# Kernel tuning notes

Measured on AMD Instinct MI355X. Metric: run time of the kernel, lower is better.

## Reference

```python
import jax, jax.numpy as jnp
import numpy as np

CAD = 5          # cubes_around_atoms_dim (default)
RES = 1.0        # resolution (default)
SIGMA = 0.93     # gaussian sigma from Li et al. 2014
LATO = 2 * CAD + 1


def _cube_offsets():
    # (LATO^3, 3) integer offsets of the neighborhood cube, as float32
    g = jnp.arange(-CAD, CAD + 1, dtype=jnp.float32)
    return jnp.stack(jnp.meshgrid(g, g, g, indexing='ij'), axis=-1).reshape(-1, 3)


def _compute_boxsize(coords):
    # Mirrors the torch code's data-dependent box sizing (concrete values).
    c = np.asarray(coords)
    minm = np.trunc(c.min(axis=1) / RES).min(axis=0)   # (3,)
    maxc = c.reshape(-1, 3).max(axis=0)                # (3,)
    return tuple(int(np.ceil(maxc[d] / RES) - minm[d] + (2 * CAD + 1)) for d in range(3))


def _forward(coords, radius, channels, numberchannels, boxsize):
    B, N, _ = coords.shape
    cube = _cube_offsets()                                   # (K,3), K = LATO^3
    mincoords = jnp.trunc(jnp.min(coords, axis=1) / RES)     # (B,3)
    translation = (mincoords - CAD)[:, None, :]              # (B,1,3)
    coords_s = coords * (1.0 / RES) - translation            # (B,N,3) scaled coords
    radius_s = radius * (1.0 / RES)                          # (B,N)
    # torch uses coords_scaled.data -> detached discrete coordinates
    disc = jnp.trunc(jax.lax.stop_gradient(coords_s))        # (B,N,3)
    # voxel centers: disc + cube + 1 + 0.5*resolution
    centers = disc[:, :, None, :] + cube[None, None] + (1.0 + 0.5 * RES)  # (B,N,K,3)
    dist = jnp.linalg.norm(coords_s[:, :, None, :] - centers, axis=-1)    # (B,N,K)
    expo = -(dist ** 2) / (SIGMA ** 2 * radius_s[:, :, None] ** 2)
    # torch clamps exponent at 10 via masked_fill (never hit: expo <= 0)
    occ = jnp.exp(jnp.minimum(expo, 10.0))                   # (B,N,K)
    idx = (disc[:, :, None, :] + cube[None, None] + 1.0).astype(jnp.int32)  # (B,N,K,3)
    b_idx = jnp.broadcast_to(jnp.arange(B, dtype=jnp.int32)[:, None, None], occ.shape)
    c_idx = jnp.broadcast_to(channels[:, :, None].astype(jnp.int32), occ.shape)
    vol = jnp.zeros((B, numberchannels) + boxsize, dtype=coords.dtype)
    vol = vol.at[b_idx.ravel(), c_idx.ravel(),
                 idx[..., 0].ravel(), idx[..., 1].ravel(), idx[..., 2].ravel()].add(occ.ravel())
    return vol


def setup_inputs() -> dict:
    key = jax.random.key(0)
    k1, k2, k3 = jax.random.split(key, 3)
    B, N, C = 4, 6000, 8
    coords = jax.random.uniform(k1, (B, N, 3), dtype=jnp.float32) * 60.0   # Angstrom box
    radius = 1.2 + 0.8 * jax.random.uniform(k2, (B, N), dtype=jnp.float32)  # vdW-like radii
    channels = jax.random.randint(k3, (B, N), 0, C)
    return {"coords": coords, "radius": radius, "channels": channels, "numberchannels": C}


def reference(coords, radius, channels, numberchannels):
    boxsize = _compute_boxsize(coords)
    return _forward(coords, radius, channels, numberchannels, boxsize)
```

## Files before the change

### kernel.cpp

```cpp
#include <hip/hip_runtime.h>


#define CAD 5
#define LATO 11
#define KOFF 1331
#define SIGMA 0.93f
#define BFIX 4
#define CFIX 8

#define RX 8
#define RY 8
#define RZ 8
#define XSTR 65
#define XCH_C (8 * XSTR)
#define SAMAX 512
#define NBB_CAP 6144

#define WS_MIN   0
#define WS_MAX   12
#define WS_CHT   24
#define WS_OFFS  64
#define WS_PACK  (WS_OFFS + BFIX * CFIX * NBB_CAP + 64)

struct Geo {
    int bx, by, bz, nbx, nby, nbz, nbb, nrx, nry, nrz;
    float tr[BFIX][3];
};

__device__ __forceinline__ void derive_geo(const float* __restrict__ ws, Geo& g) {
    float box[3];
#pragma unroll
    for (int d = 0; d < 3; ++d) {
        float lo = 1e30f, hi = -1e30f;
#pragma unroll
        for (int b = 0; b < BFIX; ++b) {
            float mnb = truncf(ws[WS_MIN + b * 3 + d]);
            lo = fminf(lo, mnb);
            hi = fmaxf(hi, ws[WS_MAX + b * 3 + d]);
            g.tr[b][d] = mnb - (float)CAD;
        }
        box[d] = ceilf(hi) - lo + (float)(2 * CAD + 1);
    }
    g.bx = (int)box[0]; g.by = (int)box[1]; g.bz = (int)box[2];
    g.nbx = (g.bx + 3) >> 2; g.nby = (g.by + 3) >> 2; g.nbz = (g.bz + 3) >> 2;
    g.nbb = g.nbx * g.nby * g.nbz;
    g.nrx = (g.bx + RX - 1) / RX;
    g.nry = (g.by + RY - 1) / RY;
    g.nrz = (g.bz + RZ - 1) / RZ;
}

__global__ __launch_bounds__(256) void vx_minmax(const float* __restrict__ coords,
                                                 const int* __restrict__ channels,
                                                 int N, float* __restrict__ ws) {
    int b = blockIdx.x;
    const float* c = coords + (size_t)b * N * 3;
    int* wsI = (int*)ws;

    __shared__ int chc[CFIX];
    if (threadIdx.x < CFIX) chc[threadIdx.x] = 0;
    __syncthreads();

    float mn[3] = {1e30f, 1e30f, 1e30f};
    float mx[3] = {-1e30f, -1e30f, -1e30f};
    for (int i = threadIdx.x; i < N; i += 256) {
#pragma unroll
        for (int d = 0; d < 3; ++d) {
            float v = c[i * 3 + d];
            mn[d] = fminf(mn[d], v);
            mx[d] = fmaxf(mx[d], v);
        }
        atomicAdd(&chc[channels[(size_t)b * N + i] & 7], 1);
    }
#pragma unroll
    for (int off = 32; off >= 1; off >>= 1) {
#pragma unroll
        for (int d = 0; d < 3; ++d) {
            mn[d] = fminf(mn[d], __shfl_down(mn[d], off, 64));
            mx[d] = fmaxf(mx[d], __shfl_down(mx[d], off, 64));
        }
    }
    __shared__ float smn[4][3], smx[4][3];
    int wave = threadIdx.x >> 6;
    if ((threadIdx.x & 63) == 0) {
#pragma unroll
        for (int d = 0; d < 3; ++d) { smn[wave][d] = mn[d]; smx[wave][d] = mx[d]; }
    }
    __syncthreads();
    if (threadIdx.x == 0) {
#pragma unroll
        for (int d = 0; d < 3; ++d) {
            for (int w = 1; w < 4; ++w) {
                mn[d] = fminf(mn[d], smn[w][d]);
                mx[d] = fmaxf(mx[d], smx[w][d]);
            }
            ws[WS_MIN + b * 3 + d] = mn[d];
            ws[WS_MAX + b * 3 + d] = mx[d];
        }
    }
    if (threadIdx.x < CFIX) wsI[WS_CHT + b * CFIX + threadIdx.x] = chc[threadIdx.x];
}

__global__ __launch_bounds__(1024) void vx_bin(const float* __restrict__ coords,
                                               const float* __restrict__ radius,
                                               const int* __restrict__ channels,
                                               float* __restrict__ ws, int N) {
    int c = blockIdx.x;
    int b = blockIdx.y;
    Geo g;
    derive_geo(ws, g);
    int* wsI = (int*)ws;
    int nbb = g.nbb;
    int t = threadIdx.x;

    __shared__ int cnt[NBB_CAP];
    __shared__ int ssum[1024];

    for (int i = t; i < nbb; i += 1024) cnt[i] = 0;
    __syncthreads();

    const float* cb = coords + (size_t)b * N * 3;
    float trx = g.tr[b][0], try_ = g.tr[b][1], trz = g.tr[b][2];

    for (int i = t; i < N; i += 1024) {
        if ((channels[(size_t)b * N + i] & 7) != c) continue;
        float sx = cb[i * 3 + 0] - trx;
        float sy = cb[i * 3 + 1] - try_;
        float sz = cb[i * 3 + 2] - trz;
        int bin = ((((int)sx) >> 2) * g.nby + (((int)sy) >> 2)) * g.nbz + (((int)sz) >> 2);
        atomicAdd(&cnt[bin], 1);
    }
    __syncthreads();

    int base = t * 6;
    int v[6];
    int sum = 0;
#pragma unroll
    for (int k = 0; k < 6; ++k) {
        v[k] = sum;
        int idx = base + k;
        sum += (idx < nbb) ? cnt[idx] : 0;
    }
    ssum[t] = sum;
    __syncthreads();
    for (int off = 1; off < 1024; off <<= 1) {
        int x = (t >= off) ? ssum[t - off] : 0;
        __syncthreads();
        ssum[t] += x;
        __syncthreads();
    }
    int excl = ssum[t] - sum;

    int gbase = b * N;
    for (int cc = 0; cc < 8; ++cc)
        if (cc < c) gbase += wsI[WS_CHT + b * CFIX + cc];

    int tab = (b * CFIX + c) * nbb;
#pragma unroll
    for (int k = 0; k < 6; ++k) {
        int idx = base + k;
        if (idx < nbb) wsI[WS_OFFS + tab + idx] = gbase + excl + v[k];
    }
    __syncthreads();
#pragma unroll
    for (int k = 0; k < 6; ++k) {
        int idx = base + k;
        if (idx < nbb) cnt[idx] = gbase + excl + v[k];
    }
    if (b == BFIX - 1 && c == CFIX - 1 && t == 0)
        wsI[WS_OFFS + BFIX * CFIX * nbb] = BFIX * N;
    __syncthreads();

    float4* p4 = (float4*)(ws + WS_PACK);
    for (int i = t; i < N; i += 1024) {
        if ((channels[(size_t)b * N + i] & 7) != c) continue;
        float sx = cb[i * 3 + 0] - trx;
        float sy = cb[i * 3 + 1] - try_;
        float sz = cb[i * 3 + 2] - trz;
        int bin = ((((int)sx) >> 2) * g.nby + (((int)sy) >> 2)) * g.nbz + (((int)sz) >> 2);
        int pos = atomicAdd(&cnt[bin], 1);
        float r_ = radius[(size_t)b * N + i];
        float inv = -1.4426950408889634f / (SIGMA * SIGMA * r_ * r_);
        p4[pos] = make_float4(sx - 0.5f, sy - 0.5f, sz - 0.5f, inv);
    }
}

#define DECL2(c) float a##c##_0 = 0.f, a##c##_1 = 0.f;
#define ACC2(c) { a##c##_0 += e0; a##c##_1 += e1; }

#define BODYF(A, c)                                                           \
    {                                                                         \
        float ddz = A.z - fzs;                                                \
        if (fabsf(ddz + 0.5f) <= 6.5f) {                                      \
            float ddx = A.x - fvx;                                            \
            float ddy = A.y - fvy;                                            \
            float s2 = __builtin_fmaf(ddx, ddx, ddy * ddy);                   \
            float e0 =                                                        \
                __builtin_amdgcn_exp2f(__builtin_fmaf(ddz, ddz, s2) * A.w);   \
            ddz -= 1.f;                                                       \
            float e1 =                                                        \
                __builtin_amdgcn_exp2f(__builtin_fmaf(ddz, ddz, s2) * A.w);   \
            ACC2(c)                                                           \
        }                                                                     \
    }

#define SWEEP_CH(c)                                                           \
    {                                                                         \
        int jb = s_roff[(c) * ncolxy], je = s_roff[((c) + 1) * ncolxy];       \
        int j = jb;                                                           \
        for (; j + 3 < je; j += 4) {                                          \
            float4 A0 = sA[j], A1 = sA[j + 1], A2 = sA[j + 2], A3 = sA[j + 3];\
            BODYF(A0, c) BODYF(A1, c) BODYF(A2, c) BODYF(A3, c)               \
        }                                                                     \
        for (; j < je; ++j) { float4 A = sA[j]; BODYF(A, c) }                 \
    }

#define XW(c, s)                                                              \
    xch[(s) * XCH_C + (2 * wave + 0) * XSTR + lyx] = a##c##_0;                \
    xch[(s) * XCH_C + (2 * wave + 1) * XSTR + lyx] = a##c##_1;

__global__ __launch_bounds__(256) void vx_gather(
    const float* __restrict__ ws, float* __restrict__ out) {
    Geo g;
    derive_geo(ws, g);
    const int* wsI = (const int*)ws;
    const float4* __restrict__ pk4 = (const float4*)(ws + WS_PACK);
    int nbb = g.nbb;
    int nbb8 = nbb * CFIX;
    int nreg = g.nrx * g.nry * g.nrz;
    int b = blockIdx.y;
    int t = threadIdx.x;
    int wave = t >> 6, lane = t & 63;
    int lx = lane >> 3, ly = lane & 7;
    int lyx = ly * 8 + lx;

    __shared__ float4 sA[SAMAX];
    __shared__ float xch[4 * XCH_C];
    __shared__ int s_beg[208], s_roff[208];
    __shared__ int wtot[4];

    for (int reg = blockIdx.x; reg < nreg; reg += gridDim.x) {
        int rz = reg % g.nrz;
        int tmp = reg / g.nrz;
        int ry = tmp % g.nry;
        int rx = tmp / g.nry;
        int X0 = rx * RX, Y0 = ry * RY, Z0 = rz * RZ;
        int zs = Z0 + 2 * wave;

        float fvx = (float)(X0 + lx);
        float fvy = (float)(Y0 + ly);
        float fzs = (float)zs;

        DECL2(0) DECL2(1) DECL2(2) DECL2(3)
        DECL2(4) DECL2(5) DECL2(6) DECL2(7)

        int xb0 = max((X0 - 6) >> 2, 0), xb1 = min((X0 + 11) >> 2, g.nbx - 1);
        int yb0 = max((Y0 - 6) >> 2, 0), yb1 = min((Y0 + 11) >> 2, g.nby - 1);
        int zb0 = max((Z0 - 6) >> 2, 0), zb1 = min((Z0 + 11) >> 2, g.nbz - 1);
        int nyr = yb1 - yb0 + 1;
        int ncolxy = (xb1 - xb0 + 1) * nyr;
        int NR = ncolxy * CFIX;

        int len = 0, beg = 0;
        if (t < NR) {
            int ch = t / ncolxy;
            int col = t - ch * ncolxy;
            int xb = xb0 + col / nyr, yb = yb0 + col % nyr;
            int keyb = ch * nbb + (xb * g.nby + yb) * g.nbz;
            beg = wsI[WS_OFFS + b * nbb8 + keyb + zb0];
            len = wsI[WS_OFFS + b * nbb8 + keyb + zb1 + 1] - beg;
        }
        int incl = len;
#pragma unroll
        for (int off = 1; off < 64; off <<= 1) {
            int v = __shfl_up(incl, off, 64);
            if (lane >= off) incl += v;
        }
        if (lane == 63) wtot[wave] = incl;
        __syncthreads();
        int addb = 0;
        for (int w = 0; w < 4; ++w)
            if (w < wave) addb += wtot[w];
        incl += addb;
        int excl = incl - len;
        if (t < NR) {
            s_beg[t] = beg;
            s_roff[t + 1] = incl;
        }
        if (t == 0) s_roff[0] = 0;
        __syncthreads();
        int S = s_roff[NR];

        if (S <= SAMAX) {
            if (t < NR) {
                for (int e = 0; e < len; ++e)
                    sA[excl + e] = pk4[beg + e];
            }
            __syncthreads();
            SWEEP_CH(0) SWEEP_CH(1) SWEEP_CH(2) SWEEP_CH(3)
            SWEEP_CH(4) SWEEP_CH(5) SWEEP_CH(6) SWEEP_CH(7)
        } else {
            __syncthreads();
            for (int r2 = 0; r2 < NR; ++r2) {
                int bg = s_beg[r2];
                int ln = s_roff[r2 + 1] - s_roff[r2];
                int c = r2 / ncolxy;
                for (int e = 0; e < ln; ++e) {
                    float4 A = pk4[bg + e];
                    float ddz = A.z - fzs;
                    if (fabsf(ddz + 0.5f) <= 6.5f) {
                        float ddx = A.x - fvx, ddy = A.y - fvy;
                        float s2 = __builtin_fmaf(ddx, ddx, ddy * ddy);
                        float e0 = __builtin_amdgcn_exp2f(
                            __builtin_fmaf(ddz, ddz, s2) * A.w);
                        ddz -= 1.f;
                        float e1 = __builtin_amdgcn_exp2f(
                            __builtin_fmaf(ddz, ddz, s2) * A.w);
                        if (c < 4) {
                            if (c < 2) { if (c == 0) ACC2(0) else ACC2(1) }
                            else       { if (c == 2) ACC2(2) else ACC2(3) }
                        } else {
                            if (c < 6) { if (c == 4) ACC2(4) else ACC2(5) }
                            else       { if (c == 6) ACC2(6) else ACC2(7) }
                        }
                    }
                }
            }
        }
        __syncthreads();

        bool interior = (X0 + RX <= g.bx) && (Y0 + RY <= g.by) && (Z0 + RZ <= g.bz);
#pragma unroll
        for (int half = 0; half < 2; ++half) {
            if (half == 0) { XW(0, 0) XW(1, 1) XW(2, 2) XW(3, 3) }
            else           { XW(4, 0) XW(5, 1) XW(6, 2) XW(7, 3) }
            __syncthreads();
            if (interior) {
#pragma unroll
                for (int k = 0; k < 8; ++k) {
                    int i = k * 256 + t;
                    int z = i & 7, y = (i >> 3) & 7, x = (i >> 6) & 7;
                    int c = (i >> 9) + half * 4;
                    out[(((size_t)(b * CFIX + c) * g.bx + X0 + x) * g.by + (Y0 + y)) *
                            (size_t)g.bz + Z0 + z] =
                        xch[(i >> 9) * XCH_C + z * XSTR + y * 8 + x];
                }
            } else {
#pragma unroll
                for (int k = 0; k < 8; ++k) {
                    int i = k * 256 + t;
                    int z = i & 7, y = (i >> 3) & 7, x = (i >> 6) & 7;
                    int c = (i >> 9) + half * 4;
                    if (X0 + x < g.bx && Y0 + y < g.by && Z0 + z < g.bz)
                        out[(((size_t)(b * CFIX + c) * g.bx + X0 + x) * g.by +
                             (Y0 + y)) * (size_t)g.bz + Z0 + z] =
                            xch[(i >> 9) * XCH_C + z * XSTR + y * 8 + x];
                }
            }
            __syncthreads();
        }
    }
}

__global__ __launch_bounds__(64) void vx_scatter(
    const float* __restrict__ coords, const float* __restrict__ radius,
    const int* __restrict__ channels, const int* __restrict__ nchan,
    const float* __restrict__ ws, int B, int N, float* __restrict__ out) {
    int atom = blockIdx.x;
    int b = atom / N;
    int lane = threadIdx.x;
    Geo g;
    derive_geo(ws, g);
    int C = *nchan;
    int bx = g.bx, by = g.by, bz = g.bz;

    float cx = coords[(size_t)atom * 3 + 0] - g.tr[b][0];
    float cy = coords[(size_t)atom * 3 + 1] - g.tr[b][1];
    float cz = coords[(size_t)atom * 3 + 2] - g.tr[b][2];
    float r = radius[atom];
    int ch = channels[atom];

    float dxf = truncf(cx), dyf = truncf(cy), dzf = truncf(cz);
    float fx = cx - dxf, fy = cy - dyf, fz = cz - dzf;
    int ix0 = (int)dxf - CAD + 1, iy0 = (int)dyf - CAD + 1, iz0 = (int)dzf - CAD + 1;
    float inv_s = 1.0f / (SIGMA * SIGMA * r * r);

    __shared__ float gg[3 * LATO];
    if (lane < 3 * LATO) {
        int dim = lane / LATO;
        int i = lane - dim * LATO;
        float f = (dim == 0) ? fx : (dim == 1 ? fy : fz);
        float d = f + ((float)CAD - 1.5f) - (float)i;
        gg[lane] = __expf(-d * d * inv_s);
    }
    __syncthreads();

    int base = (((b * C + ch) * bx + ix0) * by + iy0) * bz + iz0;
    int bybz = by * bz;
    for (int k = lane; k < KOFF; k += 64) {
        int i = k / (LATO * LATO);
        int rem = k - i * (LATO * LATO);
        int j = rem / LATO;
        int l = rem - j * LATO;
        float occ = gg[i] * gg[LATO + j] * gg[2 * LATO + l];
        atomicAdd(out + base + i * bybz + j * bz + l, occ);
    }
}

extern "C" void kernel_launch(void* const* d_in, const int* in_sizes, int n_in,
                              void* d_out, int out_size, void* d_ws, size_t ws_size,
                              hipStream_t stream) {
    const float* coords = (const float*)d_in[0];
    const float* radius = (const float*)d_in[1];
    const int* channels = (const int*)d_in[2];
    const int* nchan = (const int*)d_in[3];
    float* out = (float*)d_out;
    float* ws = (float*)d_ws;

    const int B = BFIX;
    int N = in_sizes[0] / (B * 3);
    size_t need = ((size_t)WS_PACK + (size_t)B * N * 4) * 4;

    vx_minmax<<<B, 256, 0, stream>>>(coords, channels, N, ws);

    if (ws_size >= need) {
        vx_bin<<<dim3(CFIX, B), 1024, 0, stream>>>(coords, radius, channels, ws, N);
        vx_gather<<<dim3(729, B), 256, 0, stream>>>(ws, out);
    } else {
        hipMemsetAsync(d_out, 0, (size_t)out_size * sizeof(float), stream);
        vx_scatter<<<B * N, 64, 0, stream>>>(coords, radius, channels, nchan, ws, B, N, out);
    }
}
```

Before: 82.00 us.

## Fuse min/max and channel counting into bin kernel; remap gather blocks per XCD

Drops the separate vx_minmax launch on the fast path: every vx_bin block now recomputes all batches' min/max and its own channel histogram in shared memory. This removes one kernel launch and its serial dependency. The cost is redundant reads of the coordinates by all 32 bin blocks. The gather kernel also remaps block indices so consecutive regions land on the same XCD, aiming for better L2 locality.

```diff
diff --git a/kernel.cpp b/kernel.cpp
--- a/kernel.cpp
+++ b/kernel.cpp
@@ -18,7 +18,6 @@
 
 #define WS_MIN   0
 #define WS_MAX   12
-#define WS_CHT   24
 #define WS_OFFS  64
 #define WS_PACK  (WS_OFFS + BFIX * CFIX * NBB_CAP + 64)
 
@@ -27,16 +26,16 @@
     float tr[BFIX][3];
 };
 
-__device__ __forceinline__ void derive_geo(const float* __restrict__ ws, Geo& g) {
+__device__ __forceinline__ void geo_from(const float* mnp, const float* mxp, Geo& g) {
     float box[3];
 #pragma unroll
     for (int d = 0; d < 3; ++d) {
         float lo = 1e30f, hi = -1e30f;
 #pragma unroll
         for (int b = 0; b < BFIX; ++b) {
-            float mnb = truncf(ws[WS_MIN + b * 3 + d]);
+            float mnb = truncf(mnp[b * 3 + d]);
             lo = fminf(lo, mnb);
-            hi = fmaxf(hi, ws[WS_MAX + b * 3 + d]);
+            hi = fmaxf(hi, mxp[b * 3 + d]);
             g.tr[b][d] = mnb - (float)CAD;
         }
         box[d] = ceilf(hi) - lo + (float)(2 * CAD + 1);
@@ -49,17 +48,14 @@
     g.nrz = (g.bz + RZ - 1) / RZ;
 }
 
+__device__ __forceinline__ void derive_geo(const float* __restrict__ ws, Geo& g) {
+    geo_from(ws + WS_MIN, ws + WS_MAX, g);
+}
+
 __global__ __launch_bounds__(256) void vx_minmax(const float* __restrict__ coords,
-                                                 const int* __restrict__ channels,
                                                  int N, float* __restrict__ ws) {
     int b = blockIdx.x;
     const float* c = coords + (size_t)b * N * 3;
-    int* wsI = (int*)ws;
-
-    __shared__ int chc[CFIX];
-    if (threadIdx.x < CFIX) chc[threadIdx.x] = 0;
-    __syncthreads();
-
     float mn[3] = {1e30f, 1e30f, 1e30f};
     float mx[3] = {-1e30f, -1e30f, -1e30f};
     for (int i = threadIdx.x; i < N; i += 256) {
@@ -69,7 +65,6 @@
             mn[d] = fminf(mn[d], v);
             mx[d] = fmaxf(mx[d], v);
         }
-        atomicAdd(&chc[channels[(size_t)b * N + i] & 7], 1);
     }
 #pragma unroll
     for (int off = 32; off >= 1; off >>= 1) {
@@ -97,7 +92,6 @@
             ws[WS_MAX + b * 3 + d] = mx[d];
         }
     }
-    if (threadIdx.x < CFIX) wsI[WS_CHT + b * CFIX + threadIdx.x] = chc[threadIdx.x];
 }
 
 __global__ __launch_bounds__(1024) void vx_bin(const float* __restrict__ coords,
@@ -106,23 +100,75 @@
                                                float* __restrict__ ws, int N) {
     int c = blockIdx.x;
     int b = blockIdx.y;
-    Geo g;
-    derive_geo(ws, g);
+    int t = threadIdx.x;
+    int wave = t >> 6, lane = t & 63;
     int* wsI = (int*)ws;
-    int nbb = g.nbb;
-    int t = threadIdx.x;
-
+
+    __shared__ float smin[BFIX][3], smax[BFIX][3];
+    __shared__ float wmn[16][3], wmx[16][3];
     __shared__ int cnt[NBB_CAP];
     __shared__ int ssum[1024];
+    __shared__ int chc[CFIX];
+
+#pragma unroll
+    for (int bb = 0; bb < BFIX; ++bb) {
+        const float* cb2 = coords + (size_t)bb * N * 3;
+        float mn0 = 1e30f, mn1 = 1e30f, mn2 = 1e30f;
+        float mx0 = -1e30f, mx1 = -1e30f, mx2 = -1e30f;
+        for (int i = t; i < N; i += 1024) {
+            float x = cb2[i * 3 + 0], y = cb2[i * 3 + 1], z = cb2[i * 3 + 2];
+            mn0 = fminf(mn0, x); mx0 = fmaxf(mx0, x);
+            mn1 = fminf(mn1, y); mx1 = fmaxf(mx1, y);
+            mn2 = fminf(mn2, z); mx2 = fmaxf(mx2, z);
+        }
+#pragma unroll
+        for (int off = 32; off >= 1; off >>= 1) {
+            mn0 = fminf(mn0, __shfl_down(mn0, off, 64));
+            mn1 = fminf(mn1, __shfl_down(mn1, off, 64));
+            mn2 = fminf(mn2, __shfl_down(mn2, off, 64));
+            mx0 = fmaxf(mx0, __shfl_down(mx0, off, 64));
+            mx1 = fmaxf(mx1, __shfl_down(mx1, off, 64));
+            mx2 = fmaxf(mx2, __shfl_down(mx2, off, 64));
+        }
+        if (lane == 0) {
+            wmn[wave][0] = mn0; wmn[wave][1] = mn1; wmn[wave][2] = mn2;
+            wmx[wave][0] = mx0; wmx[wave][1] = mx1; wmx[wave][2] = mx2;
+        }
+        __syncthreads();
+        if (t == 0) {
+#pragma unroll
+            for (int d = 0; d < 3; ++d) {
+                float lo = wmn[0][d], hi = wmx[0][d];
+                for (int w = 1; w < 16; ++w) {
+                    lo = fminf(lo, wmn[w][d]);
+                    hi = fmaxf(hi, wmx[w][d]);
+                }
+                smin[bb][d] = lo;
+                smax[bb][d] = hi;
+            }
+        }
+        __syncthreads();
+    }
+    if (t < 12) {
+        ws[WS_MIN + t] = smin[t / 3][t % 3];
+        ws[WS_MAX + t] = smax[t / 3][t % 3];
+    }
+
+    Geo g;
+    geo_from(&smin[0][0], &smax[0][0], g);
+    int nbb = g.nbb;
 
     for (int i = t; i < nbb; i += 1024) cnt[i] = 0;
+    if (t < CFIX) chc[t] = 0;
     __syncthreads();
 
     const float* cb = coords + (size_t)b * N * 3;
     float trx = g.tr[b][0], try_ = g.tr[b][1], trz = g.tr[b][2];
 
     for (int i = t; i < N; i += 1024) {
-        if ((channels[(size_t)b * N + i] & 7) != c) continue;
+        int ch = channels[(size_t)b * N + i] & 7;
+        atomicAdd(&chc[ch], 1);
+        if (ch != c) continue;
         float sx = cb[i * 3 + 0] - trx;
         float sy = cb[i * 3 + 1] - try_;
         float sz = cb[i * 3 + 2] - trz;
@@ -151,8 +197,8 @@
     int excl = ssum[t] - sum;
 
     int gbase = b * N;
-    for (int cc = 0; cc < 8; ++cc)
-        if (cc < c) gbase += wsI[WS_CHT + b * CFIX + cc];
+    for (int cc = 0; cc < CFIX; ++cc)
+        if (cc < c) gbase += chc[cc];
 
     int tab = (b * CFIX + c) * nbb;
 #pragma unroll
@@ -238,7 +284,12 @@
     __shared__ int s_beg[208], s_roff[208];
     __shared__ int wtot[4];
 
-    for (int reg = blockIdx.x; reg < nreg; reg += gridDim.x) {
+    int nwg = gridDim.x;
+    int q = nwg >> 3, r = nwg & 7;
+    int xcd = blockIdx.x & 7, jj = blockIdx.x >> 3;
+    int reg0 = ((xcd < r) ? xcd * (q + 1) : r * (q + 1) + (xcd - r) * q) + jj;
+
+    for (int reg = reg0; reg < nreg; reg += nwg) {
         int rz = reg % g.nrz;
         int tmp = reg / g.nrz;
         int ry = tmp % g.nry;
@@ -420,12 +471,11 @@
     int N = in_sizes[0] / (B * 3);
     size_t need = ((size_t)WS_PACK + (size_t)B * N * 4) * 4;
 
-    vx_minmax<<<B, 256, 0, stream>>>(coords, channels, N, ws);
-
     if (ws_size >= need) {
         vx_bin<<<dim3(CFIX, B), 1024, 0, stream>>>(coords, radius, channels, ws, N);
         vx_gather<<<dim3(729, B), 256, 0, stream>>>(ws, out);
     } else {
+        vx_minmax<<<B, 256, 0, stream>>>(coords, N, ws);
         hipMemsetAsync(d_out, 0, (size_t)out_size * sizeof(float), stream);
         vx_scatter<<<B * N, 64, 0, stream>>>(coords, radius, channels, nchan, ws, B, N, out);
     }
```

After: 93.23 us. +13.7%, slower.
